# Kernel optimization log

Measured on AMD Instinct MI355X. Metric: run time of the kernel, lower is better.

The kernel has to match this reference:

```python
import jax, jax.numpy as jnp
import numpy as np

B, C, H, W = 16, 512, 64, 64
G = 32            # factor; dynamic multinomial group count must equal factor for conv shapes to match
CG = C // G       # channels per group = 16
R = 16            # SE reduction
EPS = 1e-5


def setup_inputs() -> dict:
    key = jax.random.key(0)
    ks = jax.random.split(key, 8)
    n = lambda k, s: jax.random.normal(k, s, dtype=jnp.float32) * 0.05
    return {
        "x": jax.random.normal(ks[0], (B, C, H, W), dtype=jnp.float32),
        # 1x1 conv over cg channels (acts on concatenated pooled h/w strips)
        "w1": n(ks[1], (CG, CG)), "b1": jnp.zeros((CG,), jnp.float32),
        # 3x3 conv over cg channels
        "w3": n(ks[2], (CG, CG, 3, 3)), "b3": jnp.zeros((CG,), jnp.float32),
        # GroupNorm(num_groups=cg, num_channels=cg) affine -> per-channel over HW
        "gn_w": jnp.ones((CG,), jnp.float32), "gn_b": jnp.zeros((CG,), jnp.float32),
        # channel_gate SE (1x1 convs == dense on pooled vector)
        "cg_w1": n(ks[3], (C // R, C)), "cg_b1": jnp.zeros((C // R,), jnp.float32),
        "cg_w2": n(ks[4], (C, C // R)), "cg_b2": jnp.zeros((C,), jnp.float32),
        # global_attn SE
        "ga_w1": n(ks[5], (C // R, C)), "ga_b1": jnp.zeros((C // R,), jnp.float32),
        "ga_w2": n(ks[6], (C, C // R)), "ga_b2": jnp.zeros((C,), jnp.float32),
        # torch init is zeros(1); use 0.5 so the channel branch contributes to output
        "gamma": jnp.full((1,), 0.5, jnp.float32),
    }


def _se(t, wa, ba, wb, bb):
    # AdaptiveAvgPool2d(1) -> 1x1 conv -> ReLU -> 1x1 conv -> sigmoid
    p = t.mean((2, 3))                                  # (b, c)
    hdn = jax.nn.relu(p @ wa.T + ba)                    # (b, c//r)
    return jax.nn.sigmoid(hdn @ wb.T + bb)[:, :, None, None]


def reference(x, w1, b1, w3, b3, gn_w, gn_b, cg_w1, cg_b1, cg_w2, cg_b2,
              ga_w1, ga_b1, ga_w2, ga_b2, gamma):
    b, c, h, w = x.shape
    g, cg = G, c // G
    gx = x.reshape(b * g, cg, h, w)

    # coordinate pooling: (bg, cg, h, 1) and (bg, cg, w, 1)
    xh = gx.mean(3, keepdims=True)
    xw = gx.mean(2, keepdims=True).transpose(0, 1, 3, 2)
    hw = jnp.einsum('oc,bcld->bold', w1, jnp.concatenate([xh, xw], axis=2))
    hw = hw + b1[None, :, None, None]
    xh, xw = hw[:, :, :h], hw[:, :, h:]

    # gated map + per-channel GroupNorm (num_groups == num_channels)
    x1 = gx * jax.nn.sigmoid(xh) * jax.nn.sigmoid(xw.transpose(0, 1, 3, 2))
    mu = x1.mean((2, 3), keepdims=True)
    var = x1.var((2, 3), keepdims=True)
    x1 = (x1 - mu) * jax.lax.rsqrt(var + EPS)
    x1 = x1 * gn_w[None, :, None, None] + gn_b[None, :, None, None]

    # 3x3 conv branch
    x2 = jax.lax.conv_general_dilated(gx, w3, (1, 1), 'SAME',
                                      dimension_numbers=('NCHW', 'OIHW', 'NCHW'))
    x2 = x2 + b3[None, :, None, None]

    # pooled-softmax cross attention: (bg,1,cg) @ (bg,cg,hw)
    a11 = jax.nn.softmax(x1.mean((2, 3)), axis=-1)      # (bg, cg)
    a21 = jax.nn.softmax(x2.mean((2, 3)), axis=-1)
    wv = jnp.einsum('bc,bchw->bhw', a11, x2) + jnp.einsum('bc,bchw->bhw', a21, x1)
    spatial = (gx * jax.nn.sigmoid(wv)[:, None]).reshape(b, c, h, w)

    channel = x * _se(x, cg_w1, cg_b1, cg_w2, cg_b2)
    fused = spatial + gamma * channel
    return fused * _se(fused, ga_w1, ga_b1, ga_w2, ga_b2)
```

## Files before the change

### kernel.cpp

```cpp
#include <hip/hip_runtime.h>
#include <math.h>

#define EPS 1e-5f

typedef float __attribute__((ext_vector_type(4))) floatx4;

__device__ __forceinline__ float sigmoidf_(float v){ return 1.0f/(1.0f+expf(-v)); }

__global__ __launch_bounds__(1024, 4) void kA(const float* __restrict__ x,
    const float* __restrict__ w1, const float* __restrict__ b1,
    const float* __restrict__ w3, const float* __restrict__ b3,
    const float* __restrict__ gn_w, const float* __restrict__ gn_b,
    float* __restrict__ sh, float* __restrict__ sw,
    float* __restrict__ chansum, float* __restrict__ alpha, float* __restrict__ cst,
    float* __restrict__ weff, float* __restrict__ bconst)
{
    const int bg = blockIdx.x;
    const int tid = threadIdx.x;
    const int w = tid >> 6;
    const int lane = tid & 63;

    __shared__ float rs_s[16][64], cs_s[16][64];
    __shared__ float sh_s[16][64], sw_s[16][64];
    __shared__ float chs_s[16], corn_s[16][4], mu_s[16], rstd_s[16];
    __shared__ float w3s[2304], w1s[256], b1s[16];
    __shared__ float regs[144], m2[16], a21_s[16];

    for (int t=tid; t<2304; t+=1024) w3s[t] = w3[t];
    if (tid < 256) w1s[tid] = w1[tid];
    if (tid < 16)  b1s[tid] = b1[tid];

    const float4* xc4 = (const float4*)(x + (((size_t)bg<<4) + w)*4096);

    float4 xv[16];
    float c0=0.f,c1=0.f,c2=0.f,c3=0.f;
    #pragma unroll
    for (int it=0; it<16; ++it){
        float4 v = xc4[it*64 + lane];
        xv[it] = v;
        float rsum = v.x+v.y+v.z+v.w;
        rsum += __shfl_xor(rsum,1); rsum += __shfl_xor(rsum,2);
        rsum += __shfl_xor(rsum,4); rsum += __shfl_xor(rsum,8);
        if ((lane&15)==0) rs_s[w][it*4 + (lane>>4)] = rsum;
        c0+=v.x; c1+=v.y; c2+=v.z; c3+=v.w;
    }
    c0 += __shfl_xor(c0,16); c0 += __shfl_xor(c0,32);
    c1 += __shfl_xor(c1,16); c1 += __shfl_xor(c1,32);
    c2 += __shfl_xor(c2,16); c2 += __shfl_xor(c2,32);
    c3 += __shfl_xor(c3,16); c3 += __shfl_xor(c3,32);
    float tsum = c0+c1+c2+c3;
    tsum += __shfl_xor(tsum,1); tsum += __shfl_xor(tsum,2);
    tsum += __shfl_xor(tsum,4); tsum += __shfl_xor(tsum,8);
    if (lane < 16){
        cs_s[w][lane*4+0]=c0; cs_s[w][lane*4+1]=c1;
        cs_s[w][lane*4+2]=c2; cs_s[w][lane*4+3]=c3;
    }
    if (lane==0){
        chs_s[w]=tsum;
        chansum[(bg<<4)+w]=tsum;
        const float* xb = x + (((size_t)bg<<4)+w)*4096;
        corn_s[w][0]=xb[0]; corn_s[w][1]=xb[63];
        corn_s[w][2]=xb[4032]; corn_s[w][3]=xb[4095];
    }
    __syncthreads();

    {
        int p  = tid & 127;
        int o0 = tid >> 7;
        bool isrow = (p < 64);
        int pp = p & 63;
        float cat[16];
        #pragma unroll
        for (int cc=0; cc<16; ++cc)
            cat[cc] = (isrow ? rs_s[cc][pp] : cs_s[cc][pp]) * (1.0f/64.0f);
        #pragma unroll
        for (int t2=0; t2<2; ++t2){
            int o = o0 + t2*8;
            float acc = b1s[o];
            #pragma unroll
            for (int cc=0; cc<16; ++cc) acc += w1s[o*16+cc]*cat[cc];
            float sg = sigmoidf_(acc);
            if (isrow){ sh_s[o][pp]=sg; sh[bg*1024 + o*64 + pp]=sg; }
            else      { sw_s[o][pp]=sg; sw[bg*1024 + o*64 + pp]=sg; }
        }
    }
    __syncthreads();

    {
        int jb = (lane&15)*4;
        float sw0=sw_s[w][jb], sw1=sw_s[w][jb+1], sw2=sw_s[w][jb+2], sw3=sw_s[w][jb+3];
        float s1=0.f, s2=0.f;
        #pragma unroll
        for (int it=0; it<16; ++it){
            float4 v = xv[it];
            float si = sh_s[w][it*4+(lane>>4)];
            float a0=v.x*si*sw0, a1=v.y*si*sw1, a2=v.z*si*sw2, a3=v.w*si*sw3;
            s1 += a0+a1+a2+a3;
            s2 += a0*a0+a1*a1+a2*a2+a3*a3;
        }
        #pragma unroll
        for (int m=1;m<64;m<<=1){ s1+=__shfl_xor(s1,m); s2+=__shfl_xor(s2,m); }
        if (lane==0){
            float mu = s1*(1.0f/4096.0f);
            float var = s2*(1.0f/4096.0f) - mu*mu;
            mu_s[w]=mu; rstd_s[w]=rsqrtf(var+EPS);
        }
    }
    __syncthreads();

    if (tid < 144){
        int c = tid/9, k = tid - c*9, ky = k/3, kx = k - ky*3;
        float r = chs_s[c];
        if (ky==0) r -= rs_s[c][63];
        if (ky==2) r -= rs_s[c][0];
        if (kx==0) r -= cs_s[c][63];
        if (kx==2) r -= cs_s[c][0];
        if (ky!=1 && kx!=1) r += corn_s[c][((ky==0)?2:0)+((kx==0)?1:0)];
        regs[tid] = r;
    }
    __syncthreads();
    if (tid<16){
        float s=0.f;
        const float* wo = w3s + tid*144;
        for (int q=0;q<144;++q) s += wo[q]*regs[q];
        m2[tid] = b3[tid] + s*(1.0f/4096.0f);
    }
    __syncthreads();
    if (tid==0){
        float m = m2[0];
        for (int i=1;i<16;++i) m = fmaxf(m, m2[i]);
        float s=0.f, e[16];
        for (int i=0;i<16;++i){ e[i]=expf(m2[i]-m); s+=e[i]; }
        for (int i=0;i<16;++i) a21_s[i]=e[i]/s;
    }
    __syncthreads();
    if (tid<16){
        alpha[(bg<<4)+tid] = a21_s[tid]*gn_w[tid]*rstd_s[tid];
    }
    if (tid==0){
        float cv=0.f;
        for (int c2=0;c2<16;++c2)
            cv += a21_s[c2]*(gn_b[c2] - gn_w[c2]*rstd_s[c2]*mu_s[c2]);
        cst[bg]=cv;
    }

    if (bg==0 && tid<160){
        float a11[16];
        {
            float m = gn_b[0];
            #pragma unroll
            for (int i=1;i<16;++i) m = fmaxf(m, gn_b[i]);
            float s=0.f;
            #pragma unroll
            for (int i=0;i<16;++i){ a11[i]=expf(gn_b[i]-m); s+=a11[i]; }
            float inv = 1.0f/s;
            #pragma unroll
            for (int i=0;i<16;++i) a11[i]*=inv;
        }
        if (tid<144){
            float acc=0.f;
            #pragma unroll
            for (int o=0;o<16;++o) acc += a11[o]*w3s[o*144+tid];
            weff[tid]=acc;
        }
        if (tid==159){
            float acc=0.f;
            #pragma unroll
            for (int o=0;o<16;++o) acc += a11[o]*b3[o];
            bconst[0]=acc;
        }
    }
}

__global__ __launch_bounds__(256) void k5_wv(const float* __restrict__ x,
    const float* __restrict__ sh, const float* __restrict__ sw,
    const float* __restrict__ alpha, const float* __restrict__ cst,
    const float* __restrict__ weff, const float* __restrict__ bconst,
    float* __restrict__ sigbuf, float* __restrict__ p2part)
{
    const int bid = blockIdx.x;
    const int bg  = bid >> 2;
    const int quarter = bid & 3;
    const int tid = threadIdx.x;
    const int j   = tid & 63;
    const int w   = tid >> 6;
    __shared__ float red[4][16];

    const int r0 = __builtin_amdgcn_readfirstlane(quarter*16 + w*4);
    const float* xb  = x + (size_t)bg*65536;
    const float* shb = sh + bg*1024;
    const float* swb = sw + bg*1024;
    const float* alb = alpha + bg*16;
    const float cstv = cst[bg] + bconst[0];

    float A0[4], A1[4], A2[4], G[4];
    float keep[16][4];
    #pragma unroll
    for (int r=0;r<4;++r){ A0[r]=0.f; A1[r]=0.f; A2[r]=0.f; G[r]=0.f; }

    #pragma unroll
    for (int c=0;c<16;++c){
        const float* xc = xb + c*4096;
        const float* wq = weff + c*9;
        float w0=wq[0], w1_=wq[1], w2=wq[2];
        float w3_=wq[3], w4=wq[4], w5=wq[5];
        float w6=wq[6], w7=wq[7], w8=wq[8];
        float alc = alb[c];
        float swv = swb[c*64 + j];
        float v[6];
        #pragma unroll
        for (int k=0;k<6;++k){
            int t = r0 - 1 + k;
            int tc = t < 0 ? 0 : (t > 63 ? 63 : t);
            float val = xc[tc*64 + j];
            v[k] = (t >= 0 && t < 64) ? val : 0.f;
        }
        #pragma unroll
        for (int r=0;r<4;++r) keep[c][r] = v[r+1];
        #pragma unroll
        for (int k=0;k<6;++k){
            if (k<=3){ A0[k]+=w0*v[k]; A1[k]+=w1_*v[k]; A2[k]+=w2*v[k]; }
            if (k>=1 && k<=4){
                A0[k-1]+=w3_*v[k]; A1[k-1]+=w4*v[k]; A2[k-1]+=w5*v[k];
                float u = alc * shb[c*64 + (r0+k-1)];
                G[k-1] += u * (swv * v[k]);
            }
            if (k>=2){ A0[k-2]+=w6*v[k]; A1[k-2]+=w7*v[k]; A2[k-2]+=w8*v[k]; }
        }
    }

    float sg[4];
    #pragma unroll
    for (int r=0;r<4;++r){
        float l = __shfl_up(A0[r], 1);
        if (j==0) l = 0.f;
        float rr = __shfl_down(A2[r], 1);
        if (j==63) rr = 0.f;
        float s = sigmoidf_(l + A1[r] + rr + G[r] + cstv);
        sg[r] = s;
        sigbuf[bg*4096 + (r0+r)*64 + j] = s;
    }

    #pragma unroll
    for (int c=0;c<16;++c){
        float acc = keep[c][0]*sg[0] + keep[c][1]*sg[1]
                  + keep[c][2]*sg[2] + keep[c][3]*sg[3];
        #pragma unroll
        for (int m=1;m<64;m<<=1) acc += __shfl_xor(acc, m);
        if (j==0) red[w][c] = acc;
    }
    __syncthreads();
    if (tid<16){
        p2part[bid*16 + tid] = red[0][tid]+red[1][tid]+red[2][tid]+red[3][tid];
    }
}

__global__ __launch_bounds__(512) void k_se12(const float* __restrict__ chansum,
    const float* __restrict__ p2part, const float* __restrict__ gamma,
    const float* __restrict__ cg_w1, const float* __restrict__ cg_b1,
    const float* __restrict__ cg_w2, const float* __restrict__ cg_b2,
    const float* __restrict__ ga_w1, const float* __restrict__ ga_b1,
    const float* __restrict__ ga_w2, const float* __restrict__ ga_b2,
    float* __restrict__ se1, float* __restrict__ se2)
{
    int b = blockIdx.x, tid = threadIdx.x;
    __shared__ float pv[512];
    __shared__ float hdn[32];
    __shared__ float se1_s[512];

    float cs_v = chansum[b*512+tid];
    pv[tid] = cs_v*(1.0f/4096.0f);
    __syncthreads();
    if (tid<32){
        float acc = cg_b1[tid];
        const float* wr = cg_w1 + tid*512;
        for (int k=0;k<512;++k) acc += wr[k]*pv[k];
        hdn[tid] = fmaxf(acc, 0.0f);
    }
    __syncthreads();
    {
        float acc = cg_b2[tid];
        const float* wr = cg_w2 + tid*32;
        #pragma unroll
        for (int k=0;k<32;++k) acc += wr[k]*hdn[k];
        float s1v = sigmoidf_(acc);
        se1_s[tid] = s1v;
        se1[b*512+tid] = s1v;
    }
    __syncthreads();

    {
        int bg = b*32 + (tid>>4);
        int c  = tid & 15;
        float praw = p2part[(bg*4+0)*16 + c] + p2part[(bg*4+1)*16 + c]
                   + p2part[(bg*4+2)*16 + c] + p2part[(bg*4+3)*16 + c];
        float g0 = gamma[0];
        pv[tid] = (praw + g0*se1_s[tid]*cs_v) * (1.0f/4096.0f);
    }
    __syncthreads();

    if (tid<32){
        float acc = ga_b1[tid];
        const float* wr = ga_w1 + tid*512;
        for (int k=0;k<512;++k) acc += wr[k]*pv[k];
        hdn[tid] = fmaxf(acc, 0.0f);
    }
    __syncthreads();
    {
        float acc = ga_b2[tid];
        const float* wr = ga_w2 + tid*32;
        #pragma unroll
        for (int k=0;k<32;++k) acc += wr[k]*hdn[k];
        se2[b*512+tid] = sigmoidf_(acc);
    }
}

__global__ __launch_bounds__(256) void k7_out(const float* __restrict__ x,
    const float* __restrict__ sigbuf, const float* __restrict__ se1,
    const float* __restrict__ se2, const float* __restrict__ gamma,
    float* __restrict__ out)
{
    const floatx4* x4 = (const floatx4*)x;
    const floatx4* s4 = (const floatx4*)sigbuf;
    floatx4* o4 = (floatx4*)out;
    float g0 = gamma[0];
    int idx = blockIdx.x*256 + threadIdx.x;
    int stride = gridDim.x*256;
    for (int g4 = idx; g4 < 8388608; g4 += stride){
        int e = g4 << 2;
        int bC = e >> 12;
        int pix4 = g4 & 1023;
        int bg = bC >> 4;
        floatx4 xv = x4[g4];
        floatx4 sg = s4[bg*1024 + pix4];
        float f1 = g0*se1[bC];
        float s2v = se2[bC];
        floatx4 ov;
        ov.x = xv.x*(sg.x+f1)*s2v;
        ov.y = xv.y*(sg.y+f1)*s2v;
        ov.z = xv.z*(sg.z+f1)*s2v;
        ov.w = xv.w*(sg.w+f1)*s2v;
        __builtin_nontemporal_store(ov, &o4[g4]);
    }
}

extern "C" void kernel_launch(void* const* d_in, const int* in_sizes, int n_in,
                              void* d_out, int out_size, void* d_ws, size_t ws_size,
                              hipStream_t stream)
{
    const float* x     = (const float*)d_in[0];
    const float* w1    = (const float*)d_in[1];
    const float* b1    = (const float*)d_in[2];
    const float* w3    = (const float*)d_in[3];
    const float* b3    = (const float*)d_in[4];
    const float* gn_w  = (const float*)d_in[5];
    const float* gn_b  = (const float*)d_in[6];
    const float* cg_w1 = (const float*)d_in[7];
    const float* cg_b1 = (const float*)d_in[8];
    const float* cg_w2 = (const float*)d_in[9];
    const float* cg_b2 = (const float*)d_in[10];
    const float* ga_w1 = (const float*)d_in[11];
    const float* ga_b1 = (const float*)d_in[12];
    const float* ga_w2 = (const float*)d_in[13];
    const float* ga_b2 = (const float*)d_in[14];
    const float* gamma = (const float*)d_in[15];
    float* out = (float*)d_out;
    float* ws  = (float*)d_ws;

    float* sh      = ws + 0;
    float* sw      = ws + 524288;
    float* chansum = ws + 1048576;
    float* alpha   = ws + 1056768;
    float* cst     = ws + 1064960;
    float* weff    = ws + 1065472;
    float* bconst  = ws + 1065616;
    float* sigbuf  = ws + 1065728;
    float* p2part  = ws + 3162880;
    float* se1     = ws + 3195648;
    float* se2     = ws + 3203840;

    kA<<<512,1024,0,stream>>>(x, w1, b1, w3, b3, gn_w, gn_b, sh, sw, chansum, alpha, cst, weff, bconst);
    k5_wv<<<2048,256,0,stream>>>(x, sh, sw, alpha, cst, weff, bconst, sigbuf, p2part);
    k_se12<<<16,512,0,stream>>>(chansum, p2part, gamma, cg_w1, cg_b1, cg_w2, cg_b2,
                                ga_w1, ga_b1, ga_w2, ga_b2, se1, se2);
    k7_out<<<8192,256,0,stream>>>(x, sigbuf, se1, se2, gamma, out);
}
```

Measured before the change: 147.3 us.

## Fuse pooling/stats kernel with 3x3 conv and wv kernel, keeping x in registers

Result: slower. 283.7 us (+92.5%).

```diff
diff --git a/kernel.cpp b/kernel.cpp
--- a/kernel.cpp
+++ b/kernel.cpp
@@ -7,61 +7,65 @@
 
 __device__ __forceinline__ float sigmoidf_(float v){ return 1.0f/(1.0f+expf(-v)); }
 
-__global__ __launch_bounds__(1024, 4) void kA(const float* __restrict__ x,
+__global__ __launch_bounds__(1024, 4) void kAB(const float* __restrict__ x,
     const float* __restrict__ w1, const float* __restrict__ b1,
     const float* __restrict__ w3, const float* __restrict__ b3,
     const float* __restrict__ gn_w, const float* __restrict__ gn_b,
-    float* __restrict__ sh, float* __restrict__ sw,
-    float* __restrict__ chansum, float* __restrict__ alpha, float* __restrict__ cst,
-    float* __restrict__ weff, float* __restrict__ bconst)
+    float* __restrict__ chansum, float* __restrict__ sigbuf, float* __restrict__ p2part)
 {
     const int bg = blockIdx.x;
     const int tid = threadIdx.x;
     const int w = tid >> 6;
     const int lane = tid & 63;
+    const int g = lane >> 4;
+    const int m = lane & 15;
 
     __shared__ float rs_s[16][64], cs_s[16][64];
     __shared__ float sh_s[16][64], sw_s[16][64];
     __shared__ float chs_s[16], corn_s[16][4], mu_s[16], rstd_s[16];
     __shared__ float w3s[2304], w1s[256], b1s[16];
     __shared__ float regs[144], m2[16], a21_s[16];
+    __shared__ float weff_s[144], alpha_s[16], cb_s[2];
+    __shared__ float wv[4096];
 
     for (int t=tid; t<2304; t+=1024) w3s[t] = w3[t];
     if (tid < 256) w1s[tid] = w1[tid];
     if (tid < 16)  b1s[tid] = b1[tid];
-
-    const float4* xc4 = (const float4*)(x + (((size_t)bg<<4) + w)*4096);
+    wv[tid*4+0]=0.f; wv[tid*4+1]=0.f; wv[tid*4+2]=0.f; wv[tid*4+3]=0.f;
+
+    const float* xc = x + (((size_t)bg<<4) + w)*4096;
+    const float4* xc4 = (const float4*)xc;
 
     float4 xv[16];
+    #pragma unroll
+    for (int q=0;q<16;++q) xv[q] = xc4[(g*16+q)*16 + m];
+
     float c0=0.f,c1=0.f,c2=0.f,c3=0.f;
     #pragma unroll
-    for (int it=0; it<16; ++it){
-        float4 v = xc4[it*64 + lane];
-        xv[it] = v;
+    for (int q=0;q<16;++q){
+        float4 v = xv[q];
         float rsum = v.x+v.y+v.z+v.w;
         rsum += __shfl_xor(rsum,1); rsum += __shfl_xor(rsum,2);
         rsum += __shfl_xor(rsum,4); rsum += __shfl_xor(rsum,8);
-        if ((lane&15)==0) rs_s[w][it*4 + (lane>>4)] = rsum;
+        if (m==0) rs_s[w][16*g+q] = rsum;
         c0+=v.x; c1+=v.y; c2+=v.z; c3+=v.w;
     }
     c0 += __shfl_xor(c0,16); c0 += __shfl_xor(c0,32);
     c1 += __shfl_xor(c1,16); c1 += __shfl_xor(c1,32);
     c2 += __shfl_xor(c2,16); c2 += __shfl_xor(c2,32);
     c3 += __shfl_xor(c3,16); c3 += __shfl_xor(c3,32);
+    if (g==0){
+        cs_s[w][4*m+0]=c0; cs_s[w][4*m+1]=c1;
+        cs_s[w][4*m+2]=c2; cs_s[w][4*m+3]=c3;
+    }
     float tsum = c0+c1+c2+c3;
     tsum += __shfl_xor(tsum,1); tsum += __shfl_xor(tsum,2);
     tsum += __shfl_xor(tsum,4); tsum += __shfl_xor(tsum,8);
-    if (lane < 16){
-        cs_s[w][lane*4+0]=c0; cs_s[w][lane*4+1]=c1;
-        cs_s[w][lane*4+2]=c2; cs_s[w][lane*4+3]=c3;
-    }
-    if (lane==0){
-        chs_s[w]=tsum;
-        chansum[(bg<<4)+w]=tsum;
-        const float* xb = x + (((size_t)bg<<4)+w)*4096;
-        corn_s[w][0]=xb[0]; corn_s[w][1]=xb[63];
-        corn_s[w][2]=xb[4032]; corn_s[w][3]=xb[4095];
-    }
+    if (lane==0){ chs_s[w]=tsum; chansum[(bg<<4)+w]=tsum; }
+    if (lane==0)  corn_s[w][0]=xv[0].x;
+    if (lane==15) corn_s[w][1]=xv[0].w;
+    if (lane==48) corn_s[w][2]=xv[15].x;
+    if (lane==63) corn_s[w][3]=xv[15].w;
     __syncthreads();
 
     {
@@ -80,26 +84,50 @@
             #pragma unroll
             for (int cc=0; cc<16; ++cc) acc += w1s[o*16+cc]*cat[cc];
             float sg = sigmoidf_(acc);
-            if (isrow){ sh_s[o][pp]=sg; sh[bg*1024 + o*64 + pp]=sg; }
-            else      { sw_s[o][pp]=sg; sw[bg*1024 + o*64 + pp]=sg; }
-        }
-    }
-    __syncthreads();
-
-    {
-        int jb = (lane&15)*4;
-        float sw0=sw_s[w][jb], sw1=sw_s[w][jb+1], sw2=sw_s[w][jb+2], sw3=sw_s[w][jb+3];
+            if (isrow) sh_s[o][pp]=sg;
+            else       sw_s[o][pp]=sg;
+        }
+    }
+    if (tid < 145){
+        float a11[16];
+        {
+            float mx = gn_b[0];
+            #pragma unroll
+            for (int i=1;i<16;++i) mx = fmaxf(mx, gn_b[i]);
+            float s=0.f;
+            #pragma unroll
+            for (int i=0;i<16;++i){ a11[i]=expf(gn_b[i]-mx); s+=a11[i]; }
+            float inv = 1.0f/s;
+            #pragma unroll
+            for (int i=0;i<16;++i) a11[i]*=inv;
+        }
+        if (tid<144){
+            float acc=0.f;
+            #pragma unroll
+            for (int o=0;o<16;++o) acc += a11[o]*w3s[o*144+tid];
+            weff_s[tid]=acc;
+        } else {
+            float acc=0.f;
+            #pragma unroll
+            for (int o=0;o<16;++o) acc += a11[o]*b3[o];
+            cb_s[1]=acc;
+        }
+    }
+    __syncthreads();
+
+    {
+        float4 swv4 = *(const float4*)&sw_s[w][4*m];
         float s1=0.f, s2=0.f;
         #pragma unroll
-        for (int it=0; it<16; ++it){
-            float4 v = xv[it];
-            float si = sh_s[w][it*4+(lane>>4)];
-            float a0=v.x*si*sw0, a1=v.y*si*sw1, a2=v.z*si*sw2, a3=v.w*si*sw3;
+        for (int q=0;q<16;++q){
+            float si = sh_s[w][16*g+q];
+            float a0=xv[q].x*si*swv4.x, a1=xv[q].y*si*swv4.y;
+            float a2=xv[q].z*si*swv4.z, a3=xv[q].w*si*swv4.w;
             s1 += a0+a1+a2+a3;
             s2 += a0*a0+a1*a1+a2*a2+a3*a3;
         }
         #pragma unroll
-        for (int m=1;m<64;m<<=1){ s1+=__shfl_xor(s1,m); s2+=__shfl_xor(s2,m); }
+        for (int mm=1;mm<64;mm<<=1){ s1+=__shfl_xor(s1,mm); s2+=__shfl_xor(s2,mm); }
         if (lane==0){
             float mu = s1*(1.0f/4096.0f);
             float var = s2*(1.0f/4096.0f) - mu*mu;
@@ -127,131 +155,100 @@
     }
     __syncthreads();
     if (tid==0){
-        float m = m2[0];
-        for (int i=1;i<16;++i) m = fmaxf(m, m2[i]);
+        float mx = m2[0];
+        for (int i=1;i<16;++i) mx = fmaxf(mx, m2[i]);
         float s=0.f, e[16];
-        for (int i=0;i<16;++i){ e[i]=expf(m2[i]-m); s+=e[i]; }
+        for (int i=0;i<16;++i){ e[i]=expf(m2[i]-mx); s+=e[i]; }
         for (int i=0;i<16;++i) a21_s[i]=e[i]/s;
     }
     __syncthreads();
-    if (tid<16){
-        alpha[(bg<<4)+tid] = a21_s[tid]*gn_w[tid]*rstd_s[tid];
-    }
+    if (tid<16) alpha_s[tid] = a21_s[tid]*gn_w[tid]*rstd_s[tid];
     if (tid==0){
         float cv=0.f;
         for (int c2=0;c2<16;++c2)
             cv += a21_s[c2]*(gn_b[c2] - gn_w[c2]*rstd_s[c2]*mu_s[c2]);
-        cst[bg]=cv;
-    }
-
-    if (bg==0 && tid<160){
-        float a11[16];
-        {
-            float m = gn_b[0];
-            #pragma unroll
-            for (int i=1;i<16;++i) m = fmaxf(m, gn_b[i]);
-            float s=0.f;
-            #pragma unroll
-            for (int i=0;i<16;++i){ a11[i]=expf(gn_b[i]-m); s+=a11[i]; }
-            float inv = 1.0f/s;
-            #pragma unroll
-            for (int i=0;i<16;++i) a11[i]*=inv;
-        }
-        if (tid<144){
-            float acc=0.f;
-            #pragma unroll
-            for (int o=0;o<16;++o) acc += a11[o]*w3s[o*144+tid];
-            weff[tid]=acc;
-        }
-        if (tid==159){
-            float acc=0.f;
-            #pragma unroll
-            for (int o=0;o<16;++o) acc += a11[o]*b3[o];
-            bconst[0]=acc;
-        }
-    }
-}
-
-__global__ __launch_bounds__(256) void k5_wv(const float* __restrict__ x,
-    const float* __restrict__ sh, const float* __restrict__ sw,
-    const float* __restrict__ alpha, const float* __restrict__ cst,
-    const float* __restrict__ weff, const float* __restrict__ bconst,
-    float* __restrict__ sigbuf, float* __restrict__ p2part)
-{
-    const int bid = blockIdx.x;
-    const int bg  = bid >> 2;
-    const int quarter = bid & 3;
-    const int tid = threadIdx.x;
-    const int j   = tid & 63;
-    const int w   = tid >> 6;
-    __shared__ float red[4][16];
-
-    const int r0 = __builtin_amdgcn_readfirstlane(quarter*16 + w*4);
-    const float* xb  = x + (size_t)bg*65536;
-    const float* shb = sh + bg*1024;
-    const float* swb = sw + bg*1024;
-    const float* alb = alpha + bg*16;
-    const float cstv = cst[bg] + bconst[0];
-
-    float A0[4], A1[4], A2[4], G[4];
-    float keep[16][4];
-    #pragma unroll
-    for (int r=0;r<4;++r){ A0[r]=0.f; A1[r]=0.f; A2[r]=0.f; G[r]=0.f; }
-
-    #pragma unroll
-    for (int c=0;c<16;++c){
-        const float* xc = xb + c*4096;
-        const float* wq = weff + c*9;
-        float w0=wq[0], w1_=wq[1], w2=wq[2];
-        float w3_=wq[3], w4=wq[4], w5=wq[5];
-        float w6=wq[6], w7=wq[7], w8=wq[8];
-        float alc = alb[c];
-        float swv = swb[c*64 + j];
-        float v[6];
-        #pragma unroll
-        for (int k=0;k<6;++k){
-            int t = r0 - 1 + k;
-            int tc = t < 0 ? 0 : (t > 63 ? 63 : t);
-            float val = xc[tc*64 + j];
-            v[k] = (t >= 0 && t < 64) ? val : 0.f;
-        }
-        #pragma unroll
-        for (int r=0;r<4;++r) keep[c][r] = v[r+1];
-        #pragma unroll
-        for (int k=0;k<6;++k){
-            if (k<=3){ A0[k]+=w0*v[k]; A1[k]+=w1_*v[k]; A2[k]+=w2*v[k]; }
-            if (k>=1 && k<=4){
-                A0[k-1]+=w3_*v[k]; A1[k-1]+=w4*v[k]; A2[k-1]+=w5*v[k];
-                float u = alc * shb[c*64 + (r0+k-1)];
-                G[k-1] += u * (swv * v[k]);
-            }
-            if (k>=2){ A0[k-2]+=w6*v[k]; A1[k-2]+=w7*v[k]; A2[k-2]+=w8*v[k]; }
-        }
-    }
-
-    float sg[4];
-    #pragma unroll
-    for (int r=0;r<4;++r){
-        float l = __shfl_up(A0[r], 1);
-        if (j==0) l = 0.f;
-        float rr = __shfl_down(A2[r], 1);
-        if (j==63) rr = 0.f;
-        float s = sigmoidf_(l + A1[r] + rr + G[r] + cstv);
-        sg[r] = s;
-        sigbuf[bg*4096 + (r0+r)*64 + j] = s;
-    }
-
-    #pragma unroll
-    for (int c=0;c<16;++c){
-        float acc = keep[c][0]*sg[0] + keep[c][1]*sg[1]
-                  + keep[c][2]*sg[2] + keep[c][3]*sg[3];
-        #pragma unroll
-        for (int m=1;m<64;m<<=1) acc += __shfl_xor(acc, m);
-        if (j==0) red[w][c] = acc;
-    }
-    __syncthreads();
-    if (tid<16){
-        p2part[bid*16 + tid] = red[0][tid]+red[1][tid]+red[2][tid]+red[3][tid];
+        cb_s[0]=cv;
+    }
+    __syncthreads();
+
+    {
+        const float al = alpha_s[w];
+        float cw0=weff_s[w*9+0], cw1=weff_s[w*9+1], cw2=weff_s[w*9+2];
+        float cw3=weff_s[w*9+3], cw4=weff_s[w*9+4], cw5=weff_s[w*9+5];
+        float cw6=weff_s[w*9+6], cw7=weff_s[w*9+7], cw8=weff_s[w*9+8];
+        float4 swv4 = *(const float4*)&sw_s[w][4*m];
+
+        float4 upH, dnH;
+        upH.x=__shfl(xv[15].x,lane-16); upH.y=__shfl(xv[15].y,lane-16);
+        upH.z=__shfl(xv[15].z,lane-16); upH.w=__shfl(xv[15].w,lane-16);
+        dnH.x=__shfl(xv[0].x,lane+16);  dnH.y=__shfl(xv[0].y,lane+16);
+        dnH.z=__shfl(xv[0].z,lane+16);  dnH.w=__shfl(xv[0].w,lane+16);
+        if (g==0){ upH.x=0.f;upH.y=0.f;upH.z=0.f;upH.w=0.f; }
+        if (g==3){ dnH.x=0.f;dnH.y=0.f;dnH.z=0.f;dnH.w=0.f; }
+
+        float4 rp = upH, rc = xv[0];
+        float Lp = __shfl(rp.w, lane-1); if (m==0)  Lp=0.f;
+        float Rp = __shfl(rp.x, lane+1); if (m==15) Rp=0.f;
+        float Lc = __shfl(rc.w, lane-1); if (m==0)  Lc=0.f;
+        float Rc = __shfl(rc.x, lane+1); if (m==15) Rc=0.f;
+
+        #pragma unroll
+        for (int q=0;q<16;++q){
+            float4 rn = (q<15) ? xv[q+1] : dnH;
+            float Ln = __shfl(rn.w, lane-1); if (m==0)  Ln=0.f;
+            float Rn = __shfl(rn.x, lane+1); if (m==15) Rn=0.f;
+
+            float t = al * sh_s[w][16*g+q];
+            float o0 = cw0*Lp   + cw1*rp.x + cw2*rp.y
+                     + cw3*Lc   + cw4*rc.x + cw5*rc.y
+                     + cw6*Ln   + cw7*rn.x + cw8*rn.y + t*swv4.x*rc.x;
+            float o1 = cw0*rp.x + cw1*rp.y + cw2*rp.z
+                     + cw3*rc.x + cw4*rc.y + cw5*rc.z
+                     + cw6*rn.x + cw7*rn.y + cw8*rn.z + t*swv4.y*rc.y;
+            float o2 = cw0*rp.y + cw1*rp.z + cw2*rp.w
+                     + cw3*rc.y + cw4*rc.z + cw5*rc.w
+                     + cw6*rn.y + cw7*rn.z + cw8*rn.w + t*swv4.z*rc.z;
+            float o3 = cw0*rp.z + cw1*rp.w + cw2*Rp
+                     + cw3*rc.z + cw4*rc.w + cw5*Rc
+                     + cw6*rn.z + cw7*rn.w + cw8*Rn + t*swv4.w*rc.w;
+
+            int base = (16*g+q)*64 + 4*m;
+            atomicAdd(&wv[base+0], o0);
+            atomicAdd(&wv[base+1], o1);
+            atomicAdd(&wv[base+2], o2);
+            atomicAdd(&wv[base+3], o3);
+
+            rp=rc; Lp=Lc; Rp=Rc;
+            rc=rn; Lc=Ln; Rc=Rn;
+        }
+    }
+    __syncthreads();
+
+    {
+        const float cstv = cb_s[0] + cb_s[1];
+        int row = 4*w + g;
+        int col = 4*m;
+        float4 t = *(float4*)&wv[row*64+col];
+        float4 sg;
+        sg.x = sigmoidf_(t.x + cstv);
+        sg.y = sigmoidf_(t.y + cstv);
+        sg.z = sigmoidf_(t.z + cstv);
+        sg.w = sigmoidf_(t.w + cstv);
+        *(float4*)&wv[row*64+col] = sg;
+        *(float4*)&sigbuf[(size_t)bg*4096 + row*64+col] = sg;
+    }
+    __syncthreads();
+
+    {
+        float acc = 0.f;
+        #pragma unroll
+        for (int q=0;q<16;++q){
+            float4 s = *(const float4*)&wv[(16*g+q)*64 + 4*m];
+            acc += xv[q].x*s.x + xv[q].y*s.y + xv[q].z*s.z + xv[q].w*s.w;
+        }
+        #pragma unroll
+        for (int mm=1;mm<64;mm<<=1) acc += __shfl_xor(acc, mm);
+        if (lane==0) p2part[(bg<<4)+w] = acc;
     }
 }
 
@@ -288,17 +285,12 @@
         se1[b*512+tid] = s1v;
     }
     __syncthreads();
-
-    {
-        int bg = b*32 + (tid>>4);
-        int c  = tid & 15;
-        float praw = p2part[(bg*4+0)*16 + c] + p2part[(bg*4+1)*16 + c]
-                   + p2part[(bg*4+2)*16 + c] + p2part[(bg*4+3)*16 + c];
+    {
+        float praw = p2part[b*512+tid];
         float g0 = gamma[0];
         pv[tid] = (praw + g0*se1_s[tid]*cs_v) * (1.0f/4096.0f);
     }
     __syncthreads();
-
     if (tid<32){
         float acc = ga_b1[tid];
         const float* wr = ga_w1 + tid*512;
@@ -367,20 +359,13 @@
     float* out = (float*)d_out;
     float* ws  = (float*)d_ws;
 
-    float* sh      = ws + 0;
-    float* sw      = ws + 524288;
-    float* chansum = ws + 1048576;
-    float* alpha   = ws + 1056768;
-    float* cst     = ws + 1064960;
-    float* weff    = ws + 1065472;
-    float* bconst  = ws + 1065616;
-    float* sigbuf  = ws + 1065728;
-    float* p2part  = ws + 3162880;
-    float* se1     = ws + 3195648;
-    float* se2     = ws + 3203840;
-
-    kA<<<512,1024,0,stream>>>(x, w1, b1, w3, b3, gn_w, gn_b, sh, sw, chansum, alpha, cst, weff, bconst);
-    k5_wv<<<2048,256,0,stream>>>(x, sh, sw, alpha, cst, weff, bconst, sigbuf, p2part);
+    float* chansum = ws + 0;
+    float* p2part  = ws + 8192;
+    float* se1     = ws + 16384;
+    float* se2     = ws + 24576;
+    float* sigbuf  = ws + 32768;
+
+    kAB<<<512,1024,0,stream>>>(x, w1, b1, w3, b3, gn_w, gn_b, chansum, sigbuf, p2part);
     k_se12<<<16,512,0,stream>>>(chansum, p2part, gamma, cg_w1, cg_b1, cg_w2, cg_b2,
                                 ga_w1, ga_b1, ga_w2, ga_b2, se1, se2);
     k7_out<<<8192,256,0,stream>>>(x, sigbuf, se1, se2, gamma, out);
```

## Fuse group statistics and 3x3 conv attention kernels into one per-group kernel

Applied to the files above, without the earlier changes.

After: 169.7 us. 1.15x slower.

```diff
diff --git a/kernel.cpp b/kernel.cpp
--- a/kernel.cpp
+++ b/kernel.cpp
@@ -7,13 +7,11 @@
 
 __device__ __forceinline__ float sigmoidf_(float v){ return 1.0f/(1.0f+expf(-v)); }
 
-__global__ __launch_bounds__(1024, 4) void kA(const float* __restrict__ x,
+__global__ __launch_bounds__(1024, 4) void kAB2(const float* __restrict__ x,
     const float* __restrict__ w1, const float* __restrict__ b1,
     const float* __restrict__ w3, const float* __restrict__ b3,
     const float* __restrict__ gn_w, const float* __restrict__ gn_b,
-    float* __restrict__ sh, float* __restrict__ sw,
-    float* __restrict__ chansum, float* __restrict__ alpha, float* __restrict__ cst,
-    float* __restrict__ weff, float* __restrict__ bconst)
+    float* __restrict__ chansum, float* __restrict__ sigbuf, float* __restrict__ p2part)
 {
     const int bg = blockIdx.x;
     const int tid = threadIdx.x;
@@ -25,42 +23,44 @@
     __shared__ float chs_s[16], corn_s[16][4], mu_s[16], rstd_s[16];
     __shared__ float w3s[2304], w1s[256], b1s[16];
     __shared__ float regs[144], m2[16], a21_s[16];
+    __shared__ float weff_s[144], alpha_s[16], cb_s[2];
+    __shared__ float red_s[16][16];
 
     for (int t=tid; t<2304; t+=1024) w3s[t] = w3[t];
     if (tid < 256) w1s[tid] = w1[tid];
     if (tid < 16)  b1s[tid] = b1[tid];
 
-    const float4* xc4 = (const float4*)(x + (((size_t)bg<<4) + w)*4096);
-
-    float4 xv[16];
-    float c0=0.f,c1=0.f,c2=0.f,c3=0.f;
-    #pragma unroll
-    for (int it=0; it<16; ++it){
-        float4 v = xc4[it*64 + lane];
-        xv[it] = v;
-        float rsum = v.x+v.y+v.z+v.w;
-        rsum += __shfl_xor(rsum,1); rsum += __shfl_xor(rsum,2);
-        rsum += __shfl_xor(rsum,4); rsum += __shfl_xor(rsum,8);
-        if ((lane&15)==0) rs_s[w][it*4 + (lane>>4)] = rsum;
-        c0+=v.x; c1+=v.y; c2+=v.z; c3+=v.w;
-    }
-    c0 += __shfl_xor(c0,16); c0 += __shfl_xor(c0,32);
-    c1 += __shfl_xor(c1,16); c1 += __shfl_xor(c1,32);
-    c2 += __shfl_xor(c2,16); c2 += __shfl_xor(c2,32);
-    c3 += __shfl_xor(c3,16); c3 += __shfl_xor(c3,32);
-    float tsum = c0+c1+c2+c3;
-    tsum += __shfl_xor(tsum,1); tsum += __shfl_xor(tsum,2);
-    tsum += __shfl_xor(tsum,4); tsum += __shfl_xor(tsum,8);
-    if (lane < 16){
-        cs_s[w][lane*4+0]=c0; cs_s[w][lane*4+1]=c1;
-        cs_s[w][lane*4+2]=c2; cs_s[w][lane*4+3]=c3;
-    }
-    if (lane==0){
-        chs_s[w]=tsum;
-        chansum[(bg<<4)+w]=tsum;
-        const float* xb = x + (((size_t)bg<<4)+w)*4096;
-        corn_s[w][0]=xb[0]; corn_s[w][1]=xb[63];
-        corn_s[w][2]=xb[4032]; corn_s[w][3]=xb[4095];
+    const float* xc = x + (((size_t)bg<<4) + w)*4096;
+    const float4* xc4 = (const float4*)xc;
+
+    {
+        float c0=0.f,c1=0.f,c2=0.f,c3=0.f;
+        #pragma unroll
+        for (int it=0; it<16; ++it){
+            float4 v = xc4[it*64 + lane];
+            float rsum = v.x+v.y+v.z+v.w;
+            rsum += __shfl_xor(rsum,1); rsum += __shfl_xor(rsum,2);
+            rsum += __shfl_xor(rsum,4); rsum += __shfl_xor(rsum,8);
+            if ((lane&15)==0) rs_s[w][it*4 + (lane>>4)] = rsum;
+            c0+=v.x; c1+=v.y; c2+=v.z; c3+=v.w;
+        }
+        c0 += __shfl_xor(c0,16); c0 += __shfl_xor(c0,32);
+        c1 += __shfl_xor(c1,16); c1 += __shfl_xor(c1,32);
+        c2 += __shfl_xor(c2,16); c2 += __shfl_xor(c2,32);
+        c3 += __shfl_xor(c3,16); c3 += __shfl_xor(c3,32);
+        float tsum = c0+c1+c2+c3;
+        tsum += __shfl_xor(tsum,1); tsum += __shfl_xor(tsum,2);
+        tsum += __shfl_xor(tsum,4); tsum += __shfl_xor(tsum,8);
+        if (lane < 16){
+            cs_s[w][lane*4+0]=c0; cs_s[w][lane*4+1]=c1;
+            cs_s[w][lane*4+2]=c2; cs_s[w][lane*4+3]=c3;
+        }
+        if (lane==0){
+            chs_s[w]=tsum;
+            chansum[(bg<<4)+w]=tsum;
+            corn_s[w][0]=xc[0]; corn_s[w][1]=xc[63];
+            corn_s[w][2]=xc[4032]; corn_s[w][3]=xc[4095];
+        }
     }
     __syncthreads();
 
@@ -80,8 +80,33 @@
             #pragma unroll
             for (int cc=0; cc<16; ++cc) acc += w1s[o*16+cc]*cat[cc];
             float sg = sigmoidf_(acc);
-            if (isrow){ sh_s[o][pp]=sg; sh[bg*1024 + o*64 + pp]=sg; }
-            else      { sw_s[o][pp]=sg; sw[bg*1024 + o*64 + pp]=sg; }
+            if (isrow) sh_s[o][pp]=sg;
+            else       sw_s[o][pp]=sg;
+        }
+    }
+    if (tid < 145){
+        float a11[16];
+        {
+            float mx = gn_b[0];
+            #pragma unroll
+            for (int i=1;i<16;++i) mx = fmaxf(mx, gn_b[i]);
+            float s=0.f;
+            #pragma unroll
+            for (int i=0;i<16;++i){ a11[i]=expf(gn_b[i]-mx); s+=a11[i]; }
+            float inv = 1.0f/s;
+            #pragma unroll
+            for (int i=0;i<16;++i) a11[i]*=inv;
+        }
+        if (tid<144){
+            float acc=0.f;
+            #pragma unroll
+            for (int o=0;o<16;++o) acc += a11[o]*w3s[o*144+tid];
+            weff_s[tid]=acc;
+        } else {
+            float acc=0.f;
+            #pragma unroll
+            for (int o=0;o<16;++o) acc += a11[o]*b3[o];
+            cb_s[1]=acc;
         }
     }
     __syncthreads();
@@ -92,14 +117,14 @@
         float s1=0.f, s2=0.f;
         #pragma unroll
         for (int it=0; it<16; ++it){
-            float4 v = xv[it];
+            float4 v = xc4[it*64+lane];
             float si = sh_s[w][it*4+(lane>>4)];
             float a0=v.x*si*sw0, a1=v.y*si*sw1, a2=v.z*si*sw2, a3=v.w*si*sw3;
             s1 += a0+a1+a2+a3;
             s2 += a0*a0+a1*a1+a2*a2+a3*a3;
         }
         #pragma unroll
-        for (int m=1;m<64;m<<=1){ s1+=__shfl_xor(s1,m); s2+=__shfl_xor(s2,m); }
+        for (int mm=1;mm<64;mm<<=1){ s1+=__shfl_xor(s1,mm); s2+=__shfl_xor(s2,mm); }
         if (lane==0){
             float mu = s1*(1.0f/4096.0f);
             float var = s2*(1.0f/4096.0f) - mu*mu;
@@ -127,131 +152,90 @@
     }
     __syncthreads();
     if (tid==0){
-        float m = m2[0];
-        for (int i=1;i<16;++i) m = fmaxf(m, m2[i]);
+        float mx = m2[0];
+        for (int i=1;i<16;++i) mx = fmaxf(mx, m2[i]);
         float s=0.f, e[16];
-        for (int i=0;i<16;++i){ e[i]=expf(m2[i]-m); s+=e[i]; }
+        for (int i=0;i<16;++i){ e[i]=expf(m2[i]-mx); s+=e[i]; }
         for (int i=0;i<16;++i) a21_s[i]=e[i]/s;
     }
     __syncthreads();
-    if (tid<16){
-        alpha[(bg<<4)+tid] = a21_s[tid]*gn_w[tid]*rstd_s[tid];
-    }
+    if (tid<16) alpha_s[tid] = a21_s[tid]*gn_w[tid]*rstd_s[tid];
     if (tid==0){
         float cv=0.f;
         for (int c2=0;c2<16;++c2)
             cv += a21_s[c2]*(gn_b[c2] - gn_w[c2]*rstd_s[c2]*mu_s[c2]);
-        cst[bg]=cv;
-    }
-
-    if (bg==0 && tid<160){
-        float a11[16];
-        {
-            float m = gn_b[0];
-            #pragma unroll
-            for (int i=1;i<16;++i) m = fmaxf(m, gn_b[i]);
-            float s=0.f;
-            #pragma unroll
-            for (int i=0;i<16;++i){ a11[i]=expf(gn_b[i]-m); s+=a11[i]; }
-            float inv = 1.0f/s;
-            #pragma unroll
-            for (int i=0;i<16;++i) a11[i]*=inv;
-        }
-        if (tid<144){
-            float acc=0.f;
-            #pragma unroll
-            for (int o=0;o<16;++o) acc += a11[o]*w3s[o*144+tid];
-            weff[tid]=acc;
-        }
-        if (tid==159){
-            float acc=0.f;
-            #pragma unroll
-            for (int o=0;o<16;++o) acc += a11[o]*b3[o];
-            bconst[0]=acc;
-        }
-    }
-}
-
-__global__ __launch_bounds__(256) void k5_wv(const float* __restrict__ x,
-    const float* __restrict__ sh, const float* __restrict__ sw,
-    const float* __restrict__ alpha, const float* __restrict__ cst,
-    const float* __restrict__ weff, const float* __restrict__ bconst,
-    float* __restrict__ sigbuf, float* __restrict__ p2part)
-{
-    const int bid = blockIdx.x;
-    const int bg  = bid >> 2;
-    const int quarter = bid & 3;
-    const int tid = threadIdx.x;
-    const int j   = tid & 63;
-    const int w   = tid >> 6;
-    __shared__ float red[4][16];
-
-    const int r0 = __builtin_amdgcn_readfirstlane(quarter*16 + w*4);
-    const float* xb  = x + (size_t)bg*65536;
-    const float* shb = sh + bg*1024;
-    const float* swb = sw + bg*1024;
-    const float* alb = alpha + bg*16;
-    const float cstv = cst[bg] + bconst[0];
-
-    float A0[4], A1[4], A2[4], G[4];
-    float keep[16][4];
-    #pragma unroll
-    for (int r=0;r<4;++r){ A0[r]=0.f; A1[r]=0.f; A2[r]=0.f; G[r]=0.f; }
-
-    #pragma unroll
-    for (int c=0;c<16;++c){
-        const float* xc = xb + c*4096;
-        const float* wq = weff + c*9;
-        float w0=wq[0], w1_=wq[1], w2=wq[2];
-        float w3_=wq[3], w4=wq[4], w5=wq[5];
-        float w6=wq[6], w7=wq[7], w8=wq[8];
-        float alc = alb[c];
-        float swv = swb[c*64 + j];
-        float v[6];
-        #pragma unroll
-        for (int k=0;k<6;++k){
-            int t = r0 - 1 + k;
-            int tc = t < 0 ? 0 : (t > 63 ? 63 : t);
-            float val = xc[tc*64 + j];
-            v[k] = (t >= 0 && t < 64) ? val : 0.f;
-        }
-        #pragma unroll
-        for (int r=0;r<4;++r) keep[c][r] = v[r+1];
-        #pragma unroll
-        for (int k=0;k<6;++k){
-            if (k<=3){ A0[k]+=w0*v[k]; A1[k]+=w1_*v[k]; A2[k]+=w2*v[k]; }
-            if (k>=1 && k<=4){
-                A0[k-1]+=w3_*v[k]; A1[k-1]+=w4*v[k]; A2[k-1]+=w5*v[k];
-                float u = alc * shb[c*64 + (r0+k-1)];
-                G[k-1] += u * (swv * v[k]);
+        cb_s[0]=cv;
+    }
+    __syncthreads();
+
+    {
+        const int j = lane;
+        const int r0 = __builtin_amdgcn_readfirstlane(4*w);
+        const float* xb = x + ((size_t)bg<<4)*4096;
+        const float cstv = cb_s[0] + cb_s[1];
+
+        float A0[4], A1[4], A2[4], G[4];
+        float keep[16][4];
+        #pragma unroll
+        for (int r=0;r<4;++r){ A0[r]=0.f; A1[r]=0.f; A2[r]=0.f; G[r]=0.f; }
+
+        #pragma unroll
+        for (int c=0;c<16;++c){
+            const float* xcc = xb + c*4096;
+            float w0=weff_s[c*9+0], w1_=weff_s[c*9+1], w2=weff_s[c*9+2];
+            float w3_=weff_s[c*9+3], w4=weff_s[c*9+4], w5=weff_s[c*9+5];
+            float w6=weff_s[c*9+6], w7=weff_s[c*9+7], w8=weff_s[c*9+8];
+            float alc = alpha_s[c];
+            float swv = sw_s[c][j];
+            float v[6];
+            #pragma unroll
+            for (int k=0;k<6;++k){
+                int t = r0 - 1 + k;
+                int tc = t < 0 ? 0 : (t > 63 ? 63 : t);
+                float val = xcc[tc*64 + j];
+                v[k] = (t >= 0 && t < 64) ? val : 0.f;
             }
-            if (k>=2){ A0[k-2]+=w6*v[k]; A1[k-2]+=w7*v[k]; A2[k-2]+=w8*v[k]; }
-        }
-    }
-
-    float sg[4];
-    #pragma unroll
-    for (int r=0;r<4;++r){
-        float l = __shfl_up(A0[r], 1);
-        if (j==0) l = 0.f;
-        float rr = __shfl_down(A2[r], 1);
-        if (j==63) rr = 0.f;
-        float s = sigmoidf_(l + A1[r] + rr + G[r] + cstv);
-        sg[r] = s;
-        sigbuf[bg*4096 + (r0+r)*64 + j] = s;
-    }
-
-    #pragma unroll
-    for (int c=0;c<16;++c){
-        float acc = keep[c][0]*sg[0] + keep[c][1]*sg[1]
-                  + keep[c][2]*sg[2] + keep[c][3]*sg[3];
-        #pragma unroll
-        for (int m=1;m<64;m<<=1) acc += __shfl_xor(acc, m);
-        if (j==0) red[w][c] = acc;
+            #pragma unroll
+            for (int r=0;r<4;++r) keep[c][r] = v[r+1];
+            #pragma unroll
+            for (int k=0;k<6;++k){
+                if (k<=3){ A0[k]+=w0*v[k]; A1[k]+=w1_*v[k]; A2[k]+=w2*v[k]; }
+                if (k>=1 && k<=4){
+                    A0[k-1]+=w3_*v[k]; A1[k-1]+=w4*v[k]; A2[k-1]+=w5*v[k];
+                    float u = alc * sh_s[c][r0+k-1];
+                    G[k-1] += u * (swv * v[k]);
+                }
+                if (k>=2){ A0[k-2]+=w6*v[k]; A1[k-2]+=w7*v[k]; A2[k-2]+=w8*v[k]; }
+            }
+        }
+
+        float sg[4];
+        #pragma unroll
+        for (int r=0;r<4;++r){
+            float l = __shfl_up(A0[r], 1);
+            if (j==0) l = 0.f;
+            float rr = __shfl_down(A2[r], 1);
+            if (j==63) rr = 0.f;
+            float s = sigmoidf_(l + A1[r] + rr + G[r] + cstv);
+            sg[r] = s;
+            sigbuf[(size_t)bg*4096 + (r0+r)*64 + j] = s;
+        }
+
+        #pragma unroll
+        for (int c=0;c<16;++c){
+            float acc = keep[c][0]*sg[0] + keep[c][1]*sg[1]
+                      + keep[c][2]*sg[2] + keep[c][3]*sg[3];
+            #pragma unroll
+            for (int mm=1;mm<64;mm<<=1) acc += __shfl_xor(acc, mm);
+            if (j==0) red_s[w][c] = acc;
+        }
     }
     __syncthreads();
     if (tid<16){
-        p2part[bid*16 + tid] = red[0][tid]+red[1][tid]+red[2][tid]+red[3][tid];
+        float tot = 0.f;
+        #pragma unroll
+        for (int ww=0;ww<16;++ww) tot += red_s[ww][tid];
+        p2part[(bg<<4)+tid] = tot;
     }
 }
 
@@ -288,17 +272,12 @@
         se1[b*512+tid] = s1v;
     }
     __syncthreads();
-
-    {
-        int bg = b*32 + (tid>>4);
-        int c  = tid & 15;
-        float praw = p2part[(bg*4+0)*16 + c] + p2part[(bg*4+1)*16 + c]
-                   + p2part[(bg*4+2)*16 + c] + p2part[(bg*4+3)*16 + c];
+    {
+        float praw = p2part[b*512+tid];
         float g0 = gamma[0];
         pv[tid] = (praw + g0*se1_s[tid]*cs_v) * (1.0f/4096.0f);
     }
     __syncthreads();
-
     if (tid<32){
         float acc = ga_b1[tid];
         const float* wr = ga_w1 + tid*512;
@@ -367,20 +346,13 @@
     float* out = (float*)d_out;
     float* ws  = (float*)d_ws;
 
-    float* sh      = ws + 0;
-    float* sw      = ws + 524288;
-    float* chansum = ws + 1048576;
-    float* alpha   = ws + 1056768;
-    float* cst     = ws + 1064960;
-    float* weff    = ws + 1065472;
-    float* bconst  = ws + 1065616;
-    float* sigbuf  = ws + 1065728;
-    float* p2part  = ws + 3162880;
-    float* se1     = ws + 3195648;
-    float* se2     = ws + 3203840;
-
-    kA<<<512,1024,0,stream>>>(x, w1, b1, w3, b3, gn_w, gn_b, sh, sw, chansum, alpha, cst, weff, bconst);
-    k5_wv<<<2048,256,0,stream>>>(x, sh, sw, alpha, cst, weff, bconst, sigbuf, p2part);
+    float* chansum = ws + 0;
+    float* p2part  = ws + 8192;
+    float* se1     = ws + 16384;
+    float* se2     = ws + 24576;
+    float* sigbuf  = ws + 32768;
+
+    kAB2<<<512,1024,0,stream>>>(x, w1, b1, w3, b3, gn_w, gn_b, chansum, sigbuf, p2part);
     k_se12<<<16,512,0,stream>>>(chansum, p2part, gamma, cg_w1, cg_b1, cg_w2, cg_b2,
                                 ga_w1, ga_b1, ga_w2, ga_b2, se1, se2);
     k7_out<<<8192,256,0,stream>>>(x, sigbuf, se1, se2, gamma, out);
```
